# Optimization experiments

Hardware: AMD Instinct MI355X
Metric: run time of the kernel (lower is better)

Reference implementation:

```python
import jax, jax.numpy as jnp
import numpy as np

N = 1_000_000   # nodes in graph
F = 128         # input feature dim
H = 128         # hidden dim per layer
B = 4096        # minibatch of target nodes
S1 = 10         # fanout at layer 2 (sampling_size[1])
S0 = 25         # fanout at layer 1 (sampling_size[0])


def setup_inputs() -> dict:
    key = jax.random.key(0)
    ks = jax.random.split(key, 6)
    features = jax.random.normal(ks[0], (N, F), jnp.float32)
    nodes = jax.random.randint(ks[1], (B,), 0, N)                 # target nodes B[K]
    nbr1 = jax.random.randint(ks[2], (B, S1), 0, N)               # sampled nbrs of targets
    nbr0 = jax.random.randint(ks[3], (B, 1 + S1, S0), 0, N)       # sampled nbrs of level-1 nodes
    W0 = jax.random.normal(ks[4], (H, 2 * F), jnp.float32) * (1.0 / np.sqrt(2 * F))
    b0 = jnp.zeros((H,), jnp.float32)
    W1 = jax.random.normal(ks[5], (H, 2 * H), jnp.float32) * (1.0 / np.sqrt(2 * H))
    b1 = jnp.zeros((H,), jnp.float32)
    return dict(features=features, W0=W0, b0=b0, W1=W1, b1=b1,
                nodes=nodes, nbr1=nbr1, nbr0=nbr0)


def _l2norm(h):
    # F.normalize(h, p=2, dim=-1) with eps clamp
    n = jnp.linalg.norm(h, axis=-1, keepdims=True)
    return h / jnp.maximum(n, 1e-12)


def reference(features, W0, b0, W1, b1, nodes, nbr1, nbr0):
    # level-1 node set: each target plus its sampled neighbors -> [B, 1+S1]
    lvl1 = jnp.concatenate([nodes[:, None], nbr1], axis=1)
    # layer 1: h^1_u = norm(relu(W0 @ [h0_u ; mean(h0_nbrs)]))
    h0_self = features[lvl1]                       # [B, 1+S1, F] gather
    h0_nbr = features[nbr0].mean(axis=2)           # [B, 1+S1, S0, F] -> mean -> [B,1+S1,F]
    h1 = _l2norm(jax.nn.relu(
        jnp.concatenate([h0_self, h0_nbr], axis=-1) @ W0.T + b0))   # [B, 1+S1, H]
    # layer 2: aggregate level-1 reps of sampled neighbors of each target
    cat2 = jnp.concatenate([h1[:, 0, :], h1[:, 1:, :].mean(axis=1)], axis=-1)  # [B, 2H]
    z = _l2norm(jax.nn.relu(cat2 @ W1.T + b1))     # [B, H]
    return z
```

## Files before the change

kernel.cpp:

```cpp
#include <hip/hip_runtime.h>

#define S0V 25
#define S1V 10
#define NBATCH 4096
#define FDIM 128
#define L1N (NBATCH * 11)

typedef __attribute__((ext_vector_type(8))) short short8;
typedef __attribute__((ext_vector_type(4))) float f32x4;

__device__ __forceinline__ ushort f2bf(float f) {
  unsigned int x = __builtin_bit_cast(unsigned int, f);
  x += 0x7fffu + ((x >> 16) & 1u);
  return (ushort)(x >> 16);
}
__device__ __forceinline__ float bf2f(ushort u) {
  unsigned int x = ((unsigned int)u) << 16;
  return __builtin_bit_cast(float, x);
}

__global__ __launch_bounds__(256) void gather_mean_kernel(
    const float* __restrict__ feat, const int* __restrict__ nodes,
    const int* __restrict__ nbr1, const int* __restrict__ nbr0,
    ushort* __restrict__ Xb) {
  const int wave = threadIdx.x >> 6;
  const int lane = threadIdx.x & 63;
  const int half = lane >> 5;
  const int l = lane & 31;
  const int i = blockIdx.x * 4 + wave;
  const int b = i / 11;
  const int j = i - b * 11;
  const int self = (j == 0) ? nodes[b] : nbr1[b * S1V + (j - 1)];
  const int* nb = nbr0 + (size_t)i * S0V;

  const int myidx = nb[(lane < S0V) ? lane : 0];

  float4 acc = make_float4(0.f, 0.f, 0.f, 0.f);
#pragma unroll
  for (int k = 0; k < 12; ++k) {
    const int rr = __shfl(myidx, 2 * k + half);
    const float4 v = *(const float4*)(feat + (size_t)rr * FDIM + l * 4);
    acc.x += v.x; acc.y += v.y; acc.z += v.z; acc.w += v.w;
  }
  {
    const int rr = __shfl(myidx, 24);
    const float4 v = *(const float4*)(feat + (size_t)rr * FDIM + l * 4);
    if (half == 0) { acc.x += v.x; acc.y += v.y; acc.z += v.z; acc.w += v.w; }
  }
  acc.x += __shfl_xor(acc.x, 32);
  acc.y += __shfl_xor(acc.y, 32);
  acc.z += __shfl_xor(acc.z, 32);
  acc.w += __shfl_xor(acc.w, 32);

  const float4 sv = *(const float4*)(feat + (size_t)self * FDIM + l * 4);

  float4 val;
  if (half == 0) {
    val = sv;
  } else {
    val.x = acc.x * (1.f / 25.f); val.y = acc.y * (1.f / 25.f);
    val.z = acc.z * (1.f / 25.f); val.w = acc.w * (1.f / 25.f);
  }
  ushort4 h;
  h.x = f2bf(val.x); h.y = f2bf(val.y); h.z = f2bf(val.z); h.w = f2bf(val.w);
  *(ushort4*)(Xb + (size_t)i * 256 + half * 128 + l * 4) = h;
}

template <int OUT_BF16>
__global__ __launch_bounds__(256) void gemm_relu_l2norm_kernel(
    const ushort* __restrict__ A, const float* __restrict__ W,
    const float* __restrict__ bias, void* __restrict__ outp, int M) {
  __shared__ ushort At[128 * 80];
  __shared__ ushort Bt[128 * 80];
  const int tid = threadIdx.x;
  const int m0 = blockIdx.x * 128;
  const int wave = tid >> 6;
  const int lane = tid & 63;
  const int q = lane >> 4;
  const int r = lane & 15;
  const int wm0 = wave * 32;

  f32x4 acc[2][8] = {};

#pragma unroll
  for (int kt = 0; kt < 4; ++kt) {
    const int k0 = kt * 64;
#pragma unroll
    for (int c = 0; c < 4; ++c) {
      const int idx = tid + c * 256;
      const int row = idx >> 3, cc = idx & 7;
      const short8 v =
          *(const short8*)(A + (size_t)(m0 + row) * 256 + k0 + cc * 8);
      *(short8*)(At + row * 80 + cc * 8) = v;
    }
#pragma unroll
    for (int c = 0; c < 8; ++c) {
      const int idx = tid + c * 256;
      const int row = idx >> 4, cc = idx & 15;
      const float4 v = *(const float4*)(W + row * 256 + k0 + cc * 4);
      ushort4 h;
      h.x = f2bf(v.x); h.y = f2bf(v.y); h.z = f2bf(v.z); h.w = f2bf(v.w);
      *(ushort4*)(Bt + row * 80 + cc * 4) = h;
    }
    __syncthreads();
#pragma unroll
    for (int kk = 0; kk < 2; ++kk) {
      const int koff = kk * 32 + q * 8;
      const short8 a0 = *(const short8*)(At + (wm0 + r) * 80 + koff);
      const short8 a1 = *(const short8*)(At + (wm0 + 16 + r) * 80 + koff);
#pragma unroll
      for (int nf = 0; nf < 8; ++nf) {
        const short8 bb = *(const short8*)(Bt + (nf * 16 + r) * 80 + koff);
        acc[0][nf] = __builtin_amdgcn_mfma_f32_16x16x32_bf16(a0, bb, acc[0][nf], 0, 0, 0);
        acc[1][nf] = __builtin_amdgcn_mfma_f32_16x16x32_bf16(a1, bb, acc[1][nf], 0, 0, 0);
      }
    }
    __syncthreads();
  }

  float bvals[8];
#pragma unroll
  for (int nf = 0; nf < 8; ++nf) bvals[nf] = bias[nf * 16 + r];

  float ss[2][4] = {};
#pragma unroll
  for (int mf = 0; mf < 2; ++mf)
#pragma unroll
    for (int nf = 0; nf < 8; ++nf)
#pragma unroll
      for (int reg = 0; reg < 4; ++reg) {
        float v = acc[mf][nf][reg] + bvals[nf];
        v = fmaxf(v, 0.f);
        acc[mf][nf][reg] = v;
        ss[mf][reg] += v * v;
      }
#pragma unroll
  for (int off = 1; off < 16; off <<= 1)
#pragma unroll
    for (int mf = 0; mf < 2; ++mf)
#pragma unroll
      for (int reg = 0; reg < 4; ++reg)
        ss[mf][reg] += __shfl_xor(ss[mf][reg], off, 16);

  float inv[2][4];
#pragma unroll
  for (int mf = 0; mf < 2; ++mf)
#pragma unroll
    for (int reg = 0; reg < 4; ++reg)
      inv[mf][reg] = 1.f / fmaxf(sqrtf(ss[mf][reg]), 1e-12f);

#pragma unroll
  for (int mf = 0; mf < 2; ++mf)
#pragma unroll
    for (int reg = 0; reg < 4; ++reg) {
      const int row = m0 + wm0 + mf * 16 + q * 4 + reg;
#pragma unroll
      for (int nf = 0; nf < 8; ++nf) {
        const int col = nf * 16 + r;
        const float v = acc[mf][nf][reg] * inv[mf][reg];
        if (OUT_BF16) {
          ((ushort*)outp)[(size_t)row * 128 + col] = f2bf(v);
        } else {
          ((float*)outp)[(size_t)row * 128 + col] = v;
        }
      }
    }
}

__global__ __launch_bounds__(256) void build_x2_kernel(
    const ushort* __restrict__ H1, ushort* __restrict__ X2) {
  const int wave = threadIdx.x >> 6;
  const int lane = threadIdx.x & 63;
  const int b = blockIdx.x * 4 + wave;
  const ushort* base = H1 + (size_t)b * 11 * 128;
  const ushort2 s = *(const ushort2*)(base + lane * 2);
  float ax = 0.f, ay = 0.f;
#pragma unroll
  for (int j = 1; j <= 10; ++j) {
    const ushort2 v = *(const ushort2*)(base + j * 128 + lane * 2);
    ax += bf2f(v.x); ay += bf2f(v.y);
  }
  ushort* out = X2 + (size_t)b * 256;
  ushort2 m;
  m.x = f2bf(ax * 0.1f); m.y = f2bf(ay * 0.1f);
  *(ushort2*)(out + lane * 2) = s;
  *(ushort2*)(out + 128 + lane * 2) = m;
}

extern "C" void kernel_launch(void* const* d_in, const int* in_sizes, int n_in,
                              void* d_out, int out_size, void* d_ws, size_t ws_size,
                              hipStream_t stream) {
  const float* feat  = (const float*)d_in[0];
  const float* W0    = (const float*)d_in[1];
  const float* b0    = (const float*)d_in[2];
  const float* W1    = (const float*)d_in[3];
  const float* b1    = (const float*)d_in[4];
  const int* nodes   = (const int*)d_in[5];
  const int* nbr1    = (const int*)d_in[6];
  const int* nbr0    = (const int*)d_in[7];
  float* out = (float*)d_out;

  ushort* Xb = (ushort*)d_ws;
  ushort* H1 = (ushort*)((char*)d_ws + 23068672);
  ushort* X2 = (ushort*)((char*)d_ws + 23068672 + 11534336);

  gather_mean_kernel<<<L1N / 4, 256, 0, stream>>>(feat, nodes, nbr1, nbr0, Xb);
  gemm_relu_l2norm_kernel<1><<<L1N / 128, 256, 0, stream>>>(Xb, W0, b0, (void*)H1, L1N);
  build_x2_kernel<<<NBATCH / 4, 256, 0, stream>>>(H1, X2);
  gemm_relu_l2norm_kernel<0><<<NBATCH / 128, 256, 0, stream>>>(X2, W1, b1, (void*)out, NBATCH);
}
```

Before: 677.4 us.

## Fuse neighbor gather-mean into layer GEMMs and pre-convert weights to bf16

Layer 1's gather-mean now writes its bf16 input tile straight into shared memory and runs the GEMM, ReLU and L2 norm in the same 512-thread block. This removes the global round trip of the intermediate activation matrix. Layer 2 likewise fuses the neighbor mean with its GEMM. A small kernel converts both weight matrices to bf16 once, so GEMM blocks no longer convert fp32 weights per tile. Each block now handles 64 rows, with the N dimension split across two wave groups and a shared-memory reduction for the row norm. This adds a barrier, and the gather loads may expose more latency because the GEMM cannot overlap them within a block.

```diff
diff --git a/kernel.cpp b/kernel.cpp
--- a/kernel.cpp
+++ b/kernel.cpp
@@ -19,172 +19,176 @@
   return __builtin_bit_cast(float, x);
 }
 
-__global__ __launch_bounds__(256) void gather_mean_kernel(
+__global__ __launch_bounds__(256) void prep_w_kernel(
+    const float* __restrict__ W0, const float* __restrict__ W1,
+    ushort* __restrict__ Wb0, ushort* __restrict__ Wb1) {
+  const int idx = blockIdx.x * 256 + threadIdx.x;
+  const int sel = idx >> 13;
+  const int k = idx & 8191;
+  const float4 v = sel ? ((const float4*)W1)[k] : ((const float4*)W0)[k];
+  ushort4 h;
+  h.x = f2bf(v.x); h.y = f2bf(v.y); h.z = f2bf(v.z); h.w = f2bf(v.w);
+  if (sel) ((ushort4*)Wb1)[k] = h; else ((ushort4*)Wb0)[k] = h;
+}
+
+template <int OUT_BF16>
+__device__ __forceinline__ void gemm_norm_64(
+    ushort* __restrict__ Xs,
+    ushort* __restrict__ Wt,
+    float* __restrict__ ssb,
+    const ushort* __restrict__ Wb, const float* __restrict__ bias,
+    void* __restrict__ outp, int row0) {
+  const int tid = threadIdx.x;
+  const int wave = tid >> 6, lane = tid & 63;
+  const int q = lane >> 4, r = lane & 15;
+  const int mf = wave & 3, ch = wave >> 2;
+
+  f32x4 acc[4] = {};
+#pragma unroll
+  for (int kt = 0; kt < 4; ++kt) {
+#pragma unroll
+    for (int p = 0; p < 2; ++p) {
+      const int idx = tid + p * 512;
+      const int row = idx >> 3, cc = idx & 7;
+      const short8 v = *(const short8*)(Wb + row * 256 + kt * 64 + cc * 8);
+      *(short8*)(Wt + row * 72 + cc * 8) = v;
+    }
+    __syncthreads();
+#pragma unroll
+    for (int kk = 0; kk < 2; ++kk) {
+      const int koff = kk * 32 + q * 8;
+      const short8 a = *(const short8*)(Xs + (mf * 16 + r) * 264 + kt * 64 + koff);
+#pragma unroll
+      for (int nf = 0; nf < 4; ++nf) {
+        const short8 bb = *(const short8*)(Wt + (ch * 64 + nf * 16 + r) * 72 + koff);
+        acc[nf] = __builtin_amdgcn_mfma_f32_16x16x32_bf16(a, bb, acc[nf], 0, 0, 0);
+      }
+    }
+    __syncthreads();
+  }
+
+  float bv[4];
+#pragma unroll
+  for (int nf = 0; nf < 4; ++nf) bv[nf] = bias[ch * 64 + nf * 16 + r];
+
+  float ss[4] = {0.f, 0.f, 0.f, 0.f};
+#pragma unroll
+  for (int nf = 0; nf < 4; ++nf)
+#pragma unroll
+    for (int reg = 0; reg < 4; ++reg) {
+      float v = acc[nf][reg] + bv[nf];
+      v = fmaxf(v, 0.f);
+      acc[nf][reg] = v;
+      ss[reg] += v * v;
+    }
+#pragma unroll
+  for (int off = 1; off < 16; off <<= 1)
+#pragma unroll
+    for (int reg = 0; reg < 4; ++reg) ss[reg] += __shfl_xor(ss[reg], off, 16);
+  if (r == 0) {
+#pragma unroll
+    for (int reg = 0; reg < 4; ++reg)
+      ssb[(mf * 16 + q * 4 + reg) * 2 + ch] = ss[reg];
+  }
+  __syncthreads();
+#pragma unroll
+  for (int reg = 0; reg < 4; ++reg) {
+    const int lrow = mf * 16 + q * 4 + reg;
+    const float tot = ssb[lrow * 2] + ssb[lrow * 2 + 1];
+    const float inv = 1.f / fmaxf(sqrtf(tot), 1e-12f);
+#pragma unroll
+    for (int nf = 0; nf < 4; ++nf) {
+      const int col = ch * 64 + nf * 16 + r;
+      const float v = acc[nf][reg] * inv;
+      if (OUT_BF16)
+        ((ushort*)outp)[(size_t)(row0 + lrow) * 128 + col] = f2bf(v);
+      else
+        ((float*)outp)[(size_t)(row0 + lrow) * 128 + col] = v;
+    }
+  }
+}
+
+__global__ __launch_bounds__(512, 4) void fused_l1_kernel(
     const float* __restrict__ feat, const int* __restrict__ nodes,
     const int* __restrict__ nbr1, const int* __restrict__ nbr0,
-    ushort* __restrict__ Xb) {
-  const int wave = threadIdx.x >> 6;
-  const int lane = threadIdx.x & 63;
-  const int half = lane >> 5;
-  const int l = lane & 31;
-  const int i = blockIdx.x * 4 + wave;
-  const int b = i / 11;
-  const int j = i - b * 11;
-  const int self = (j == 0) ? nodes[b] : nbr1[b * S1V + (j - 1)];
-  const int* nb = nbr0 + (size_t)i * S0V;
-
-  const int myidx = nb[(lane < S0V) ? lane : 0];
-
-  float4 acc = make_float4(0.f, 0.f, 0.f, 0.f);
-#pragma unroll
-  for (int k = 0; k < 12; ++k) {
-    const int rr = __shfl(myidx, 2 * k + half);
-    const float4 v = *(const float4*)(feat + (size_t)rr * FDIM + l * 4);
-    acc.x += v.x; acc.y += v.y; acc.z += v.z; acc.w += v.w;
-  }
-  {
-    const int rr = __shfl(myidx, 24);
-    const float4 v = *(const float4*)(feat + (size_t)rr * FDIM + l * 4);
-    if (half == 0) { acc.x += v.x; acc.y += v.y; acc.z += v.z; acc.w += v.w; }
-  }
-  acc.x += __shfl_xor(acc.x, 32);
-  acc.y += __shfl_xor(acc.y, 32);
-  acc.z += __shfl_xor(acc.z, 32);
-  acc.w += __shfl_xor(acc.w, 32);
-
-  const float4 sv = *(const float4*)(feat + (size_t)self * FDIM + l * 4);
-
-  float4 val;
-  if (half == 0) {
-    val = sv;
-  } else {
-    val.x = acc.x * (1.f / 25.f); val.y = acc.y * (1.f / 25.f);
-    val.z = acc.z * (1.f / 25.f); val.w = acc.w * (1.f / 25.f);
-  }
-  ushort4 h;
-  h.x = f2bf(val.x); h.y = f2bf(val.y); h.z = f2bf(val.z); h.w = f2bf(val.w);
-  *(ushort4*)(Xb + (size_t)i * 256 + half * 128 + l * 4) = h;
-}
-
-template <int OUT_BF16>
-__global__ __launch_bounds__(256) void gemm_relu_l2norm_kernel(
-    const ushort* __restrict__ A, const float* __restrict__ W,
-    const float* __restrict__ bias, void* __restrict__ outp, int M) {
-  __shared__ ushort At[128 * 80];
-  __shared__ ushort Bt[128 * 80];
+    const ushort* __restrict__ Wb0, const float* __restrict__ b0,
+    ushort* __restrict__ H1) {
+  __shared__ ushort Xs[64 * 264];
+  __shared__ ushort Wt[128 * 72];
+  __shared__ float ssb[128];
   const int tid = threadIdx.x;
-  const int m0 = blockIdx.x * 128;
-  const int wave = tid >> 6;
-  const int lane = tid & 63;
-  const int q = lane >> 4;
-  const int r = lane & 15;
-  const int wm0 = wave * 32;
-
-  f32x4 acc[2][8] = {};
-
-#pragma unroll
-  for (int kt = 0; kt < 4; ++kt) {
-    const int k0 = kt * 64;
-#pragma unroll
-    for (int c = 0; c < 4; ++c) {
-      const int idx = tid + c * 256;
-      const int row = idx >> 3, cc = idx & 7;
-      const short8 v =
-          *(const short8*)(A + (size_t)(m0 + row) * 256 + k0 + cc * 8);
-      *(short8*)(At + row * 80 + cc * 8) = v;
-    }
-#pragma unroll
-    for (int c = 0; c < 8; ++c) {
-      const int idx = tid + c * 256;
-      const int row = idx >> 4, cc = idx & 15;
-      const float4 v = *(const float4*)(W + row * 256 + k0 + cc * 4);
-      ushort4 h;
-      h.x = f2bf(v.x); h.y = f2bf(v.y); h.z = f2bf(v.z); h.w = f2bf(v.w);
-      *(ushort4*)(Bt + row * 80 + cc * 4) = h;
-    }
-    __syncthreads();
-#pragma unroll
-    for (int kk = 0; kk < 2; ++kk) {
-      const int koff = kk * 32 + q * 8;
-      const short8 a0 = *(const short8*)(At + (wm0 + r) * 80 + koff);
-      const short8 a1 = *(const short8*)(At + (wm0 + 16 + r) * 80 + koff);
-#pragma unroll
-      for (int nf = 0; nf < 8; ++nf) {
-        const short8 bb = *(const short8*)(Bt + (nf * 16 + r) * 80 + koff);
-        acc[0][nf] = __builtin_amdgcn_mfma_f32_16x16x32_bf16(a0, bb, acc[0][nf], 0, 0, 0);
-        acc[1][nf] = __builtin_amdgcn_mfma_f32_16x16x32_bf16(a1, bb, acc[1][nf], 0, 0, 0);
-      }
-    }
-    __syncthreads();
-  }
-
-  float bvals[8];
-#pragma unroll
-  for (int nf = 0; nf < 8; ++nf) bvals[nf] = bias[nf * 16 + r];
-
-  float ss[2][4] = {};
-#pragma unroll
-  for (int mf = 0; mf < 2; ++mf)
-#pragma unroll
-    for (int nf = 0; nf < 8; ++nf)
-#pragma unroll
-      for (int reg = 0; reg < 4; ++reg) {
-        float v = acc[mf][nf][reg] + bvals[nf];
-        v = fmaxf(v, 0.f);
-        acc[mf][nf][reg] = v;
-        ss[mf][reg] += v * v;
-      }
-#pragma unroll
-  for (int off = 1; off < 16; off <<= 1)
-#pragma unroll
-    for (int mf = 0; mf < 2; ++mf)
-#pragma unroll
-      for (int reg = 0; reg < 4; ++reg)
-        ss[mf][reg] += __shfl_xor(ss[mf][reg], off, 16);
-
-  float inv[2][4];
-#pragma unroll
-  for (int mf = 0; mf < 2; ++mf)
-#pragma unroll
-    for (int reg = 0; reg < 4; ++reg)
-      inv[mf][reg] = 1.f / fmaxf(sqrtf(ss[mf][reg]), 1e-12f);
-
-#pragma unroll
-  for (int mf = 0; mf < 2; ++mf)
-#pragma unroll
-    for (int reg = 0; reg < 4; ++reg) {
-      const int row = m0 + wm0 + mf * 16 + q * 4 + reg;
-#pragma unroll
-      for (int nf = 0; nf < 8; ++nf) {
-        const int col = nf * 16 + r;
-        const float v = acc[mf][nf][reg] * inv[mf][reg];
-        if (OUT_BF16) {
-          ((ushort*)outp)[(size_t)row * 128 + col] = f2bf(v);
-        } else {
-          ((float*)outp)[(size_t)row * 128 + col] = v;
-        }
-      }
-    }
-}
-
-__global__ __launch_bounds__(256) void build_x2_kernel(
-    const ushort* __restrict__ H1, ushort* __restrict__ X2) {
-  const int wave = threadIdx.x >> 6;
-  const int lane = threadIdx.x & 63;
-  const int b = blockIdx.x * 4 + wave;
-  const ushort* base = H1 + (size_t)b * 11 * 128;
-  const ushort2 s = *(const ushort2*)(base + lane * 2);
-  float ax = 0.f, ay = 0.f;
-#pragma unroll
-  for (int j = 1; j <= 10; ++j) {
-    const ushort2 v = *(const ushort2*)(base + j * 128 + lane * 2);
-    ax += bf2f(v.x); ay += bf2f(v.y);
-  }
-  ushort* out = X2 + (size_t)b * 256;
-  ushort2 m;
-  m.x = f2bf(ax * 0.1f); m.y = f2bf(ay * 0.1f);
-  *(ushort2*)(out + lane * 2) = s;
-  *(ushort2*)(out + 128 + lane * 2) = m;
+  const int wave = tid >> 6, lane = tid & 63;
+  const int half = lane >> 5, l = lane & 31;
+  const int i0 = blockIdx.x * 64;
+
+  for (int t = 0; t < 8; ++t) {
+    const int row = wave * 8 + t;
+    const int i = i0 + row;
+    const int b = i / 11;
+    const int j = i - b * 11;
+    const int self = (j == 0) ? nodes[b] : nbr1[b * S1V + (j - 1)];
+    const int myidx = nbr0[(size_t)i * S0V + ((lane < S0V) ? lane : 0)];
+
+    float4 acc = make_float4(0.f, 0.f, 0.f, 0.f);
+#pragma unroll
+    for (int k = 0; k < 12; ++k) {
+      const int rr = __shfl(myidx, 2 * k + half);
+      const float4 v = *(const float4*)(feat + (size_t)rr * FDIM + l * 4);
+      acc.x += v.x; acc.y += v.y; acc.z += v.z; acc.w += v.w;
+    }
+    {
+      const int rr = __shfl(myidx, 24);
+      const float4 v = *(const float4*)(feat + (size_t)rr * FDIM + l * 4);
+      if (half == 0) { acc.x += v.x; acc.y += v.y; acc.z += v.z; acc.w += v.w; }
+    }
+    acc.x += __shfl_xor(acc.x, 32);
+    acc.y += __shfl_xor(acc.y, 32);
+    acc.z += __shfl_xor(acc.z, 32);
+    acc.w += __shfl_xor(acc.w, 32);
+
+    const float4 sv = *(const float4*)(feat + (size_t)self * FDIM + l * 4);
+    float4 val;
+    if (half == 0) {
+      val = sv;
+    } else {
+      val.x = acc.x * (1.f / 25.f); val.y = acc.y * (1.f / 25.f);
+      val.z = acc.z * (1.f / 25.f); val.w = acc.w * (1.f / 25.f);
+    }
+    ushort4 h;
+    h.x = f2bf(val.x); h.y = f2bf(val.y); h.z = f2bf(val.z); h.w = f2bf(val.w);
+    *(ushort4*)(Xs + row * 264 + half * 128 + l * 4) = h;
+  }
+  __syncthreads();
+  gemm_norm_64<1>(Xs, Wt, ssb, Wb0, b0, (void*)H1, i0);
+}
+
+__global__ __launch_bounds__(512, 4) void fused_l2_kernel(
+    const ushort* __restrict__ H1, const ushort* __restrict__ Wb1,
+    const float* __restrict__ b1, float* __restrict__ out) {
+  __shared__ ushort Xs[64 * 264];
+  __shared__ ushort Wt[128 * 72];
+  __shared__ float ssb[128];
+  const int tid = threadIdx.x;
+  const int wave = tid >> 6, lane = tid & 63;
+  const int t0 = blockIdx.x * 64;
+
+  for (int t = 0; t < 8; ++t) {
+    const int row = wave * 8 + t;
+    const ushort* base = H1 + (size_t)(t0 + row) * 11 * 128;
+    const ushort2 s = *(const ushort2*)(base + lane * 2);
+    float ax = 0.f, ay = 0.f;
+#pragma unroll
+    for (int j = 1; j <= 10; ++j) {
+      const ushort2 v = *(const ushort2*)(base + j * 128 + lane * 2);
+      ax += bf2f(v.x); ay += bf2f(v.y);
+    }
+    *(ushort2*)(Xs + row * 264 + lane * 2) = s;
+    ushort2 m;
+    m.x = f2bf(ax * 0.1f); m.y = f2bf(ay * 0.1f);
+    *(ushort2*)(Xs + row * 264 + 128 + lane * 2) = m;
+  }
+  __syncthreads();
+  gemm_norm_64<0>(Xs, Wt, ssb, Wb1, b1, (void*)out, t0);
 }
 
 extern "C" void kernel_launch(void* const* d_in, const int* in_sizes, int n_in,
@@ -200,12 +204,11 @@
   const int* nbr0    = (const int*)d_in[7];
   float* out = (float*)d_out;
 
-  ushort* Xb = (ushort*)d_ws;
-  ushort* H1 = (ushort*)((char*)d_ws + 23068672);
-  ushort* X2 = (ushort*)((char*)d_ws + 23068672 + 11534336);
-
-  gather_mean_kernel<<<L1N / 4, 256, 0, stream>>>(feat, nodes, nbr1, nbr0, Xb);
-  gemm_relu_l2norm_kernel<1><<<L1N / 128, 256, 0, stream>>>(Xb, W0, b0, (void*)H1, L1N);
-  build_x2_kernel<<<NBATCH / 4, 256, 0, stream>>>(H1, X2);
-  gemm_relu_l2norm_kernel<0><<<NBATCH / 128, 256, 0, stream>>>(X2, W1, b1, (void*)out, NBATCH);
-}
+  ushort* Wb0 = (ushort*)d_ws;
+  ushort* Wb1 = (ushort*)((char*)d_ws + 65536);
+  ushort* H1  = (ushort*)((char*)d_ws + 131072);
+
+  prep_w_kernel<<<64, 256, 0, stream>>>(W0, W1, Wb0, Wb1);
+  fused_l1_kernel<<<L1N / 64, 512, 0, stream>>>(feat, nodes, nbr1, nbr0, Wb0, b0, H1);
+  fused_l2_kernel<<<NBATCH / 64, 512, 0, stream>>>(H1, Wb1, b1, out);
+}
```

New measurement: 670.1 us. About the same (-1.1%).
